# Optimization experiments

Hardware: AMD Instinct MI355X
Metric: run time of the kernel (lower is better)

The kernel has to match this reference:

```python
import jax, jax.numpy as jnp
import numpy as np

TOKENS = 16384
IN_F = 2048
OUT_F = 2048
RANK = 32
GROUP = 64          # int4 scale group size
PAD = 256           # token padding multiple used by the fused activation quantizer
QMAX = 7.0          # signed int4 symmetric quantization


def setup_inputs() -> dict:
    key = jax.random.key(0)
    ks = jax.random.split(key, 7)
    x = jax.random.normal(ks[0], (TOKENS, IN_F), dtype=jnp.float32)
    # packed int4 weights: two signed nibbles per int8 lane
    qweight = jax.random.randint(ks[1], (OUT_F, IN_F // 2), -128, 128, dtype=jnp.int8)
    # per-group weight scales [in//group, out], strictly positive
    wscales = jnp.abs(jax.random.normal(ks[2], (IN_F // GROUP, OUT_F), dtype=jnp.float32)) * 0.01 + 1e-4
    # activation smoothing factors, positive and near 1
    smooth_factor = jnp.abs(jax.random.normal(ks[3], (IN_F,), dtype=jnp.float32)) * 0.5 + 0.75
    bias = jax.random.normal(ks[4], (OUT_F,), dtype=jnp.float32) * 0.01
    proj_down = jax.random.normal(ks[5], (IN_F, RANK), dtype=jnp.float32) * 0.02
    proj_up = jax.random.normal(ks[6], (OUT_F, RANK), dtype=jnp.float32) * 0.02
    return {"x": x, "qweight": qweight, "wscales": wscales,
            "smooth_factor": smooth_factor, "bias": bias,
            "proj_down": proj_down, "proj_up": proj_up}


def _unpack_int4(qweight):
    # low nibble = even input channel, high nibble = odd input channel; arithmetic shifts keep sign
    low = jnp.right_shift(jnp.left_shift(qweight, 4), 4)
    high = jnpp = jnp.right_shift(qweight, 4)
    w = jnp.stack([low, high], axis=-1).reshape(qweight.shape[0], qweight.shape[1] * 2)
    return w.astype(jnp.float32)  # [out, in], values in [-8, 7]


def _forward(x, qweight, wscales, smooth_factor, bias, proj_down, proj_up):
    T = x.shape[0]
    t_pad = ((T + PAD - 1) // PAD) * PAD
    # activation smoothing
    xs = x / smooth_factor
    xs_p = jnp.pad(xs, ((0, t_pad - T), (0, 0)))
    # per-token per-64-group symmetric int4 activation quantization
    xg = xs_p.reshape(t_pad, IN_F // GROUP, GROUP)
    amax = jnp.max(jnp.abs(xg), axis=-1)                       # [Tp, G]
    ascales = jnp.where(amax > 0, amax / QMAX, jnp.float32(1.0))
    qx = jnp.clip(jnp.round(xg / ascales[..., None]), -8.0, 7.0)
    xdq = (qx * ascales[..., None]).reshape(t_pad, IN_F)       # dequantized activations
    # dequantize packed int4 weights with per-group scales
    w = _unpack_int4(qweight)                                  # [out, in]
    wdq = (w.reshape(OUT_F, IN_F // GROUP, GROUP) * wscales.T[:, :, None]).reshape(OUT_F, IN_F)
    # packed GEMM (dequantized equivalent) + fused low-rank residual + bias
    y = xdq @ wdq.T                                            # [Tp, out]
    y = y + (xs_p @ proj_down) @ proj_up.T + bias
    return y[:T]


def reference(x, qweight, wscales, smooth_factor, bias, proj_down, proj_up):
    return _forward(x, qweight, wscales, smooth_factor, bias, proj_down, proj_up)
```

## Files before the change

### kernel.cpp

```cpp
#include <hip/hip_runtime.h>

#define TOKENS 16384
#define INF 2048
#define OUTF 2048
#define NGROUP 32
#define RANK 32
#define BM 128
#define BN 128

typedef int   int32x4  __attribute__((ext_vector_type(4)));
typedef int   int32x2  __attribute__((ext_vector_type(2)));
typedef float floatx4  __attribute__((ext_vector_type(4)));
typedef short bf16x8   __attribute__((ext_vector_type(8)));

typedef __attribute__((address_space(1))) const void gconst_t;
typedef __attribute__((address_space(3))) void ldsv_t;

__device__ __forceinline__ void gload_lds16(const void* g, void* l) {
  __builtin_amdgcn_global_load_lds((gconst_t*)g, (ldsv_t*)l, 16, 0, 0);
}

__device__ __forceinline__ unsigned short f2bf(float f) {
  unsigned u = __float_as_uint(f);
  unsigned r = (u + 0x7FFFu + ((u >> 16) & 1u)) >> 16;
  return (unsigned short)r;
}

__device__ __forceinline__ unsigned unp2(int e0, int e1) {
  int l0 = ((int)((unsigned)e0 << 28)) >> 28;
  int h0 = ((int)((unsigned)e0 << 24)) >> 28;
  int l1 = ((int)((unsigned)e1 << 28)) >> 28;
  int h1 = ((int)((unsigned)e1 << 24)) >> 28;
  return (l0 & 0xFF) | ((h0 & 0xFF) << 8) | ((l1 & 0xFF) << 16) | ((h1 & 0xFF) << 24);
}

__global__ __launch_bounds__(256) void unpack_kernel(const int* __restrict__ qw,
                                                     signed char* __restrict__ wq8) {
  int idx = blockIdx.x * 256 + threadIdx.x;
  const int4* src = (const int4*)qw;
  int4 v0 = src[idx * 2 + 0];
  int4 v1 = src[idx * 2 + 1];
  int4 out;
  out.x = (int)unp2(v0.x, v0.y);
  out.y = (int)unp2(v0.z, v0.w);
  out.z = (int)unp2(v1.x, v1.y);
  out.w = (int)unp2(v1.z, v1.w);
  *(int4*)(wq8 + (size_t)idx * 16) = out;
}

__global__ __launch_bounds__(256) void prep_pdT(const float* __restrict__ pd,
                                                unsigned short* __restrict__ pdT) {
  int idx = blockIdx.x * 256 + threadIdx.x;
  int r = idx >> 11, c = idx & 2047;
  pdT[idx] = f2bf(pd[(size_t)c * RANK + r]);
}

__global__ __launch_bounds__(256) void quant_kernel(
    const float* __restrict__ x, const float* __restrict__ smooth,
    const unsigned short* __restrict__ pdT,
    signed char* __restrict__ qx8, float* __restrict__ ascalesT,
    float* __restrict__ tdown) {
  __shared__ char lds[32768];
  int tid = threadIdx.x, lane = tid & 63, wid = tid >> 6;
  int t0 = blockIdx.x * 32;
  int mi = wid >> 1, ni = wid & 1;
  floatx4 acc = {0.f, 0.f, 0.f, 0.f};

  floatx4 xv[8];
  floatx4 sm;
  int32x4 pv[4];

  auto issue_loads = [&](int kc) {
    const float* xb = x + (size_t)(t0 + wid * 8) * INF + kc * 256 + lane * 4;
#pragma unroll
    for (int r = 0; r < 8; ++r) xv[r] = *(const floatx4*)(xb + r * INF);
    sm = *(const floatx4*)(smooth + kc * 256 + lane * 4);
#pragma unroll
    for (int q = 0; q < 4; ++q) {
      int flat = tid + q * 256;
      int row = flat >> 5, c16 = flat & 31;
      pv[q] = *(const int32x4*)((const char*)pdT + (size_t)row * 4096 + kc * 512 + c16 * 16);
    }
  };

  issue_loads(0);

  for (int kc = 0; kc < 8; ++kc) {
    floatx4 rsm;
    rsm[0] = 1.0f / sm[0]; rsm[1] = 1.0f / sm[1];
    rsm[2] = 1.0f / sm[2]; rsm[3] = 1.0f / sm[3];
#pragma unroll
    for (int q = 0; q < 4; ++q) {
      int flat = tid + q * 256;
      int row = flat >> 5, c16 = flat & 31;
      int byte = (row * 512 + c16 * 16) ^ ((row & 7) << 4);
      *(int32x4*)(lds + 16384 + byte) = pv[q];
    }
#pragma unroll
    for (int r = 0; r < 8; ++r) {
      floatx4 xs;
      xs[0] = xv[r][0] * rsm[0]; xs[1] = xv[r][1] * rsm[1];
      xs[2] = xv[r][2] * rsm[2]; xs[3] = xv[r][3] * rsm[3];
      float m4 = fmaxf(fmaxf(fabsf(xs[0]), fabsf(xs[1])),
                       fmaxf(fabsf(xs[2]), fabsf(xs[3])));
      m4 = fmaxf(m4, __shfl_xor(m4, 1, 64));
      m4 = fmaxf(m4, __shfl_xor(m4, 2, 64));
      m4 = fmaxf(m4, __shfl_xor(m4, 4, 64));
      m4 = fmaxf(m4, __shfl_xor(m4, 8, 64));
      float ascale = m4 > 0.f ? m4 / 7.0f : 1.0f;
      float rq = 1.0f / ascale;
      int tok = t0 + wid * 8 + r;
      if ((lane & 15) == 0)
        ascalesT[(size_t)(kc * 4 + (lane >> 4)) * TOKENS + tok] = ascale;
      int pk = 0;
#pragma unroll
      for (int b = 0; b < 4; ++b) {
        float qf = fminf(7.f, fmaxf(-8.f, rintf(xs[b] * rq)));
        pk |= ((int)qf & 0xFF) << (8 * b);
      }
      *(int*)(qx8 + (size_t)tok * INF + kc * 256 + lane * 4) = pk;
      unsigned lo = (unsigned)f2bf(xs[0]) | ((unsigned)f2bf(xs[1]) << 16);
      unsigned hi = (unsigned)f2bf(xs[2]) | ((unsigned)f2bf(xs[3]) << 16);
      int lrow = wid * 8 + r;
      int xbyte = (lrow * 512 + lane * 8) ^ ((lrow & 7) << 4);
      int32x2 wv; wv[0] = (int)lo; wv[1] = (int)hi;
      *(int32x2*)(lds + xbyte) = wv;
    }
    __syncthreads();
    if (kc + 1 < 8) issue_loads(kc + 1);
#pragma unroll
    for (int ks = 0; ks < 8; ++ks) {
      int arow = mi * 16 + (lane & 15);
      int ab = (arow * 512 + ks * 64 + ((lane >> 4) << 4)) ^ ((arow & 7) << 4);
      bf16x8 av = *(const bf16x8*)(lds + ab);
      int brow = ni * 16 + (lane & 15);
      int bb = (brow * 512 + ks * 64 + ((lane >> 4) << 4)) ^ ((brow & 7) << 4);
      bf16x8 bv = *(const bf16x8*)(lds + 16384 + bb);
      acc = __builtin_amdgcn_mfma_f32_16x16x32_bf16(av, bv, acc, 0, 0, 0);
    }
    __syncthreads();
  }

  int trow = t0 + mi * 16 + ((lane >> 4) << 2);
  int col = ni * 16 + (lane & 15);
#pragma unroll
  for (int r = 0; r < 4; ++r)
    tdown[(size_t)(trow + r) * RANK + col] = acc[r];
}

__global__ __launch_bounds__(256, 3) void gemm_kernel(
    const signed char* __restrict__ qx8, const signed char* __restrict__ wq8,
    const float* __restrict__ ascalesT, const float* __restrict__ wscales,
    const float* __restrict__ tdown, const float* __restrict__ pu,
    const float* __restrict__ bias, float* __restrict__ y) {
  __shared__ char smem[49152];

  int tid = threadIdx.x;
  int lane = tid & 63;
  int wid = tid >> 6;
  int wr = wid >> 1, wc = wid & 1;
  int o0 = blockIdx.x * BN;
  int t0 = blockIdx.y * BM;

  floatx4 acc[4][4];
#pragma unroll
  for (int m = 0; m < 4; ++m)
#pragma unroll
    for (int n = 0; n < 4; ++n) acc[m][n] = (floatx4){0.f, 0.f, 0.f, 0.f};

  auto stage = [&](int g) {
    int bufb = (g % 3) * 16384;
#pragma unroll
    for (int i = 0; i < 2; ++i) {
      int c = tid + i * 256;
      int row = c >> 2;
      int l = (c & 3) ^ ((row >> 1) & 3);
      gload_lds16(qx8 + (size_t)(t0 + row) * INF + g * 64 + l * 16,
                  smem + bufb + (wid + i * 4) * 1024);
      gload_lds16(wq8 + (size_t)(o0 + row) * INF + g * 64 + l * 16,
                  smem + bufb + 8192 + (wid + i * 4) * 1024);
    }
  };

  int aoff[4], boff[4];
#pragma unroll
  for (int m = 0; m < 4; ++m) {
    int arow = (wr << 6) + (m << 4) + (lane & 15);
    aoff[m] = arow * 64 + ((((lane >> 4)) ^ ((arow >> 1) & 3)) << 4);
    int brow = (wc << 6) + (m << 4) + (lane & 15);
    boff[m] = 8192 + brow * 64 + ((((lane >> 4)) ^ ((brow >> 1) & 3)) << 4);
  }

  const float* asp = ascalesT + t0 + (wr << 6) + ((lane >> 4) << 2);
  const float* wsp = wscales + o0 + (wc << 6) + (lane & 15);

  floatx4 asv_pf[4];
  float wsv_pf[4];
  auto scales_pf = [&](int g) {
#pragma unroll
    for (int m = 0; m < 4; ++m)
      asv_pf[m] = *(const floatx4*)(asp + (size_t)g * TOKENS + (m << 4));
#pragma unroll
    for (int n = 0; n < 4; ++n)
      wsv_pf[n] = wsp[(size_t)g * OUTF + (n << 4)];
  };

  scales_pf(0);
  stage(0);
  stage(1);

  for (int g = 0; g < NGROUP; ++g) {
    if (g == 0)               asm volatile("s_waitcnt vmcnt(4)" ::: "memory");
    else if (g == NGROUP - 1) asm volatile("s_waitcnt vmcnt(8)" ::: "memory");
    else                      asm volatile("s_waitcnt vmcnt(12)" ::: "memory");
    __builtin_amdgcn_s_barrier();
    __builtin_amdgcn_sched_barrier(0);

    floatx4 asv[4];
    float wsv[4];
#pragma unroll
    for (int m = 0; m < 4; ++m) asv[m] = asv_pf[m];
#pragma unroll
    for (int n = 0; n < 4; ++n) wsv[n] = wsv_pf[n];

    if (g + 1 < NGROUP) scales_pf(g + 1);
    if (g + 2 < NGROUP) stage(g + 2);

    int bufb = (g % 3) * 16384;
    int32x4 af[4], bf_[4];
#pragma unroll
    for (int m = 0; m < 4; ++m) af[m] = *(const int32x4*)(smem + bufb + aoff[m]);
#pragma unroll
    for (int n = 0; n < 4; ++n) bf_[n] = *(const int32x4*)(smem + bufb + boff[n]);

    __builtin_amdgcn_s_setprio(1);
#pragma unroll
    for (int m = 0; m < 4; ++m)
#pragma unroll
      for (int n = 0; n < 4; ++n) {
        int32x4 zero = {0, 0, 0, 0};
        int32x4 d = __builtin_amdgcn_mfma_i32_16x16x64_i8(af[m], bf_[n], zero, 0, 0, 0);
        floatx4 sc;
        sc[0] = asv[m][0] * wsv[n]; sc[1] = asv[m][1] * wsv[n];
        sc[2] = asv[m][2] * wsv[n]; sc[3] = asv[m][3] * wsv[n];
        acc[m][n] += __builtin_convertvector(d, floatx4) * sc;
      }
    __builtin_amdgcn_s_setprio(0);
  }

  __syncthreads();

  unsigned short* td_lds = (unsigned short*)smem;
  unsigned short* pu_lds = (unsigned short*)(smem + 8192);
  {
    int row = tid >> 1, h = (tid & 1) * 16;
    const float* ts = tdown + (size_t)(t0 + row) * RANK + h;
    const float* ps = pu + (size_t)(o0 + row) * RANK + h;
    unsigned tw[8], pw[8];
#pragma unroll
    for (int q = 0; q < 4; ++q) {
      float4 v = *(const float4*)(ts + q * 4);
      tw[q * 2 + 0] = (unsigned)f2bf(v.x) | ((unsigned)f2bf(v.y) << 16);
      tw[q * 2 + 1] = (unsigned)f2bf(v.z) | ((unsigned)f2bf(v.w) << 16);
      float4 p = *(const float4*)(ps + q * 4);
      pw[q * 2 + 0] = (unsigned)f2bf(p.x) | ((unsigned)f2bf(p.y) << 16);
      pw[q * 2 + 1] = (unsigned)f2bf(p.z) | ((unsigned)f2bf(p.w) << 16);
    }
    int4 s0, s1;
    s0.x = (int)tw[0]; s0.y = (int)tw[1]; s0.z = (int)tw[2]; s0.w = (int)tw[3];
    s1.x = (int)tw[4]; s1.y = (int)tw[5]; s1.z = (int)tw[6]; s1.w = (int)tw[7];
    *(int4*)(td_lds + row * 32 + h) = s0;
    *(int4*)(td_lds + row * 32 + h + 8) = s1;
    s0.x = (int)pw[0]; s0.y = (int)pw[1]; s0.z = (int)pw[2]; s0.w = (int)pw[3];
    s1.x = (int)pw[4]; s1.y = (int)pw[5]; s1.z = (int)pw[6]; s1.w = (int)pw[7];
    *(int4*)(pu_lds + row * 32 + h) = s0;
    *(int4*)(pu_lds + row * 32 + h + 8) = s1;
  }
  __syncthreads();

  bf16x8 ta[4], pb4[4];
  int koff8 = (lane >> 4) << 3;
#pragma unroll
  for (int m = 0; m < 4; ++m)
    ta[m] = *(const bf16x8*)&td_lds[((wr << 6) + (m << 4) + (lane & 15)) * 32 + koff8];
#pragma unroll
  for (int n = 0; n < 4; ++n)
    pb4[n] = *(const bf16x8*)&pu_lds[((wc << 6) + (n << 4) + (lane & 15)) * 32 + koff8];

#pragma unroll
  for (int n = 0; n < 4; ++n) {
    int oc = o0 + (wc << 6) + (n << 4) + (lane & 15);
    float bv = bias[oc];
#pragma unroll
    for (int m = 0; m < 4; ++m) {
      floatx4 c = acc[m][n];
      c = __builtin_amdgcn_mfma_f32_16x16x32_bf16(ta[m], pb4[n], c, 0, 0, 0);
#pragma unroll
      for (int r = 0; r < 4; ++r) {
        int tr = t0 + (wr << 6) + (m << 4) + ((lane >> 4) << 2) + r;
        y[(size_t)tr * OUTF + oc] = c[r] + bv;
      }
    }
  }
}

extern "C" void kernel_launch(void* const* d_in, const int* in_sizes, int n_in,
                              void* d_out, int out_size, void* d_ws, size_t ws_size,
                              hipStream_t stream) {
  const float* x      = (const float*)d_in[0];
  const int*   qw     = (const int*)d_in[1];
  const float* wsc    = (const float*)d_in[2];
  const float* smooth = (const float*)d_in[3];
  const float* bias   = (const float*)d_in[4];
  const float* pd     = (const float*)d_in[5];
  const float* pu     = (const float*)d_in[6];
  float* y = (float*)d_out;

  char* ws = (char*)d_ws;
  signed char* qx8 = (signed char*)ws;
  signed char* wq8 = (signed char*)(ws + 33554432);
  float* ascalesT  = (float*)(ws + 33554432 + 4194304);
  float* tdown     = (float*)(ws + 33554432 + 4194304 + 2097152);
  unsigned short* pdT = (unsigned short*)((char*)d_out + (64u << 20));

  unpack_kernel<<<1024, 256, 0, stream>>>(qw, wq8);
  prep_pdT<<<256, 256, 0, stream>>>(pd, pdT);
  quant_kernel<<<TOKENS / 32, 256, 0, stream>>>(x, smooth, pdT, qx8, ascalesT, tdown);
  gemm_kernel<<<dim3(OUTF / BN, TOKENS / BM), 256, 0, stream>>>(
      qx8, wq8, ascalesT, wsc, tdown, pu, bias, y);
}
```

Before: 218.9 us.

## Replace int8 MFMA with pre-dequantized fp16 GEMM and split tokens in halves

Activations and weights are dequantized to fp16 in the prep kernels, with the group scales folded in, so the main GEMM runs fp16 MFMA that accumulate straight into the float accumulators. This removes the per-group scale loads and the int-to-float rescale after every int8 MFMA, but it doubles operand bytes and the number of K steps (64 steps of 32 elements instead of 32 groups). The token dimension is processed in two halves so the fp16 activation buffer fits in the existing workspace, and the GEMM grid is remapped to a 1D swizzled order for better L2 locality. fp16 rounding of the dequantized values could change numerics slightly.

```diff
diff --git a/kernel.cpp b/kernel.cpp
--- a/kernel.cpp
+++ b/kernel.cpp
@@ -1,17 +1,19 @@
 #include <hip/hip_runtime.h>
 
 #define TOKENS 16384
+#define THALF 8192
 #define INF 2048
 #define OUTF 2048
-#define NGROUP 32
 #define RANK 32
 #define BM 128
 #define BN 128
+#define NKSTEP 64
 
 typedef int   int32x4  __attribute__((ext_vector_type(4)));
 typedef int   int32x2  __attribute__((ext_vector_type(2)));
 typedef float floatx4  __attribute__((ext_vector_type(4)));
 typedef short bf16x8   __attribute__((ext_vector_type(8)));
+typedef _Float16 f16x8 __attribute__((ext_vector_type(8)));
 
 typedef __attribute__((address_space(1))) const void gconst_t;
 typedef __attribute__((address_space(3))) void ldsv_t;
@@ -26,26 +28,29 @@
   return (unsigned short)r;
 }
 
-__device__ __forceinline__ unsigned unp2(int e0, int e1) {
-  int l0 = ((int)((unsigned)e0 << 28)) >> 28;
-  int h0 = ((int)((unsigned)e0 << 24)) >> 28;
-  int l1 = ((int)((unsigned)e1 << 28)) >> 28;
-  int h1 = ((int)((unsigned)e1 << 24)) >> 28;
-  return (l0 & 0xFF) | ((h0 & 0xFF) << 8) | ((l1 & 0xFF) << 16) | ((h1 & 0xFF) << 24);
-}
-
 __global__ __launch_bounds__(256) void unpack_kernel(const int* __restrict__ qw,
-                                                     signed char* __restrict__ wq8) {
+                                                     const float* __restrict__ wsc,
+                                                     _Float16* __restrict__ wdq) {
   int idx = blockIdx.x * 256 + threadIdx.x;
-  const int4* src = (const int4*)qw;
-  int4 v0 = src[idx * 2 + 0];
-  int4 v1 = src[idx * 2 + 1];
-  int4 out;
-  out.x = (int)unp2(v0.x, v0.y);
-  out.y = (int)unp2(v0.z, v0.w);
-  out.z = (int)unp2(v1.x, v1.y);
-  out.w = (int)unp2(v1.z, v1.w);
-  *(int4*)(wq8 + (size_t)idx * 16) = out;
+  int o = idx >> 6;
+  int ch = idx & 63;
+  float ws = wsc[(size_t)(ch >> 1) * OUTF + o];
+  const int4* src = (const int4*)qw + (size_t)idx * 4;
+  _Float16* dst = wdq + (size_t)o * INF + ch * 32;
+#pragma unroll
+  for (int q = 0; q < 4; ++q) {
+    int4 v = src[q];
+    int e[4] = {v.x, v.y, v.z, v.w};
+    alignas(16) _Float16 h[8];
+#pragma unroll
+    for (int j = 0; j < 4; ++j) {
+      int lo = ((int)((unsigned)e[j] << 28)) >> 28;
+      int hi = ((int)((unsigned)e[j] << 24)) >> 28;
+      h[2 * j]     = (_Float16)((float)lo * ws);
+      h[2 * j + 1] = (_Float16)((float)hi * ws);
+    }
+    *(int4*)(dst + q * 8) = *(const int4*)h;
+  }
 }
 
 __global__ __launch_bounds__(256) void prep_pdT(const float* __restrict__ pd,
@@ -58,11 +63,10 @@
 __global__ __launch_bounds__(256) void quant_kernel(
     const float* __restrict__ x, const float* __restrict__ smooth,
     const unsigned short* __restrict__ pdT,
-    signed char* __restrict__ qx8, float* __restrict__ ascalesT,
-    float* __restrict__ tdown) {
+    _Float16* __restrict__ xdq, float* __restrict__ tdown, int tbase) {
   __shared__ char lds[32768];
   int tid = threadIdx.x, lane = tid & 63, wid = tid >> 6;
-  int t0 = blockIdx.x * 32;
+  int t0rel = blockIdx.x * 32;
   int mi = wid >> 1, ni = wid & 1;
   floatx4 acc = {0.f, 0.f, 0.f, 0.f};
 
@@ -71,7 +75,7 @@
   int32x4 pv[4];
 
   auto issue_loads = [&](int kc) {
-    const float* xb = x + (size_t)(t0 + wid * 8) * INF + kc * 256 + lane * 4;
+    const float* xb = x + (size_t)(tbase + t0rel + wid * 8) * INF + kc * 256 + lane * 4;
 #pragma unroll
     for (int r = 0; r < 8; ++r) xv[r] = *(const floatx4*)(xb + r * INF);
     sm = *(const floatx4*)(smooth + kc * 256 + lane * 4);
@@ -109,16 +113,15 @@
       m4 = fmaxf(m4, __shfl_xor(m4, 8, 64));
       float ascale = m4 > 0.f ? m4 / 7.0f : 1.0f;
       float rq = 1.0f / ascale;
-      int tok = t0 + wid * 8 + r;
-      if ((lane & 15) == 0)
-        ascalesT[(size_t)(kc * 4 + (lane >> 4)) * TOKENS + tok] = ascale;
-      int pk = 0;
+      int tokrel = t0rel + wid * 8 + r;
+      alignas(8) _Float16 hq[4];
 #pragma unroll
       for (int b = 0; b < 4; ++b) {
         float qf = fminf(7.f, fmaxf(-8.f, rintf(xs[b] * rq)));
-        pk |= ((int)qf & 0xFF) << (8 * b);
+        hq[b] = (_Float16)(qf * ascale);
       }
-      *(int*)(qx8 + (size_t)tok * INF + kc * 256 + lane * 4) = pk;
+      *(int32x2*)((char*)xdq + ((size_t)tokrel * INF + kc * 256 + lane * 4) * 2) =
+          *(const int32x2*)hq;
       unsigned lo = (unsigned)f2bf(xs[0]) | ((unsigned)f2bf(xs[1]) << 16);
       unsigned hi = (unsigned)f2bf(xs[2]) | ((unsigned)f2bf(xs[3]) << 16);
       int lrow = wid * 8 + r;
@@ -141,7 +144,7 @@
     __syncthreads();
   }
 
-  int trow = t0 + mi * 16 + ((lane >> 4) << 2);
+  int trow = tbase + t0rel + mi * 16 + ((lane >> 4) << 2);
   int col = ni * 16 + (lane & 15);
 #pragma unroll
   for (int r = 0; r < 4; ++r)
@@ -149,18 +152,21 @@
 }
 
 __global__ __launch_bounds__(256, 3) void gemm_kernel(
-    const signed char* __restrict__ qx8, const signed char* __restrict__ wq8,
-    const float* __restrict__ ascalesT, const float* __restrict__ wscales,
+    const _Float16* __restrict__ xdq, const _Float16* __restrict__ wdq,
     const float* __restrict__ tdown, const float* __restrict__ pu,
-    const float* __restrict__ bias, float* __restrict__ y) {
+    const float* __restrict__ bias, float* __restrict__ y, int tbase) {
   __shared__ char smem[49152];
 
   int tid = threadIdx.x;
   int lane = tid & 63;
   int wid = tid >> 6;
   int wr = wid >> 1, wc = wid & 1;
-  int o0 = blockIdx.x * BN;
-  int t0 = blockIdx.y * BM;
+
+  int s = blockIdx.x;
+  int s2 = (s & 7) * 128 + (s >> 3);
+  int o0 = (s2 & 15) * BN;
+  int t0rel = (s2 >> 4) * BM;
+  int t0abs = tbase + t0rel;
 
   floatx4 acc[4][4];
 #pragma unroll
@@ -175,9 +181,9 @@
       int c = tid + i * 256;
       int row = c >> 2;
       int l = (c & 3) ^ ((row >> 1) & 3);
-      gload_lds16(qx8 + (size_t)(t0 + row) * INF + g * 64 + l * 16,
+      gload_lds16((const char*)xdq + (size_t)(t0rel + row) * (INF * 2) + g * 64 + l * 16,
                   smem + bufb + (wid + i * 4) * 1024);
-      gload_lds16(wq8 + (size_t)(o0 + row) * INF + g * 64 + l * 16,
+      gload_lds16((const char*)wdq + (size_t)(o0 + row) * (INF * 2) + g * 64 + l * 16,
                   smem + bufb + 8192 + (wid + i * 4) * 1024);
     }
   };
@@ -191,60 +197,30 @@
     boff[m] = 8192 + brow * 64 + ((((lane >> 4)) ^ ((brow >> 1) & 3)) << 4);
   }
 
-  const float* asp = ascalesT + t0 + (wr << 6) + ((lane >> 4) << 2);
-  const float* wsp = wscales + o0 + (wc << 6) + (lane & 15);
-
-  floatx4 asv_pf[4];
-  float wsv_pf[4];
-  auto scales_pf = [&](int g) {
-#pragma unroll
-    for (int m = 0; m < 4; ++m)
-      asv_pf[m] = *(const floatx4*)(asp + (size_t)g * TOKENS + (m << 4));
-#pragma unroll
-    for (int n = 0; n < 4; ++n)
-      wsv_pf[n] = wsp[(size_t)g * OUTF + (n << 4)];
-  };
-
-  scales_pf(0);
   stage(0);
   stage(1);
 
-  for (int g = 0; g < NGROUP; ++g) {
-    if (g == 0)               asm volatile("s_waitcnt vmcnt(4)" ::: "memory");
-    else if (g == NGROUP - 1) asm volatile("s_waitcnt vmcnt(8)" ::: "memory");
-    else                      asm volatile("s_waitcnt vmcnt(12)" ::: "memory");
+  for (int g = 0; g < NKSTEP; ++g) {
+    if (g == NKSTEP - 1) asm volatile("s_waitcnt vmcnt(0)" ::: "memory");
+    else                 asm volatile("s_waitcnt vmcnt(4)" ::: "memory");
     __builtin_amdgcn_s_barrier();
     __builtin_amdgcn_sched_barrier(0);
 
-    floatx4 asv[4];
-    float wsv[4];
-#pragma unroll
-    for (int m = 0; m < 4; ++m) asv[m] = asv_pf[m];
-#pragma unroll
-    for (int n = 0; n < 4; ++n) wsv[n] = wsv_pf[n];
-
-    if (g + 1 < NGROUP) scales_pf(g + 1);
-    if (g + 2 < NGROUP) stage(g + 2);
+    if (g + 2 < NKSTEP) stage(g + 2);
 
     int bufb = (g % 3) * 16384;
-    int32x4 af[4], bf_[4];
-#pragma unroll
-    for (int m = 0; m < 4; ++m) af[m] = *(const int32x4*)(smem + bufb + aoff[m]);
-#pragma unroll
-    for (int n = 0; n < 4; ++n) bf_[n] = *(const int32x4*)(smem + bufb + boff[n]);
+    f16x8 af[4], bf_[4];
+#pragma unroll
+    for (int m = 0; m < 4; ++m) af[m] = *(const f16x8*)(smem + bufb + aoff[m]);
+#pragma unroll
+    for (int n = 0; n < 4; ++n) bf_[n] = *(const f16x8*)(smem + bufb + boff[n]);
 
     __builtin_amdgcn_s_setprio(1);
 #pragma unroll
     for (int m = 0; m < 4; ++m)
 #pragma unroll
-      for (int n = 0; n < 4; ++n) {
-        int32x4 zero = {0, 0, 0, 0};
-        int32x4 d = __builtin_amdgcn_mfma_i32_16x16x64_i8(af[m], bf_[n], zero, 0, 0, 0);
-        floatx4 sc;
-        sc[0] = asv[m][0] * wsv[n]; sc[1] = asv[m][1] * wsv[n];
-        sc[2] = asv[m][2] * wsv[n]; sc[3] = asv[m][3] * wsv[n];
-        acc[m][n] += __builtin_convertvector(d, floatx4) * sc;
-      }
+      for (int n = 0; n < 4; ++n)
+        acc[m][n] = __builtin_amdgcn_mfma_f32_16x16x32_f16(af[m], bf_[n], acc[m][n], 0, 0, 0);
     __builtin_amdgcn_s_setprio(0);
   }
 
@@ -254,7 +230,7 @@
   unsigned short* pu_lds = (unsigned short*)(smem + 8192);
   {
     int row = tid >> 1, h = (tid & 1) * 16;
-    const float* ts = tdown + (size_t)(t0 + row) * RANK + h;
+    const float* ts = tdown + (size_t)(t0abs + row) * RANK + h;
     const float* ps = pu + (size_t)(o0 + row) * RANK + h;
     unsigned tw[8], pw[8];
 #pragma unroll
@@ -297,7 +273,7 @@
       c = __builtin_amdgcn_mfma_f32_16x16x32_bf16(ta[m], pb4[n], c, 0, 0, 0);
 #pragma unroll
       for (int r = 0; r < 4; ++r) {
-        int tr = t0 + (wr << 6) + (m << 4) + ((lane >> 4) << 2) + r;
+        int tr = t0abs + (wr << 6) + (m << 4) + ((lane >> 4) << 2) + r;
         y[(size_t)tr * OUTF + oc] = c[r] + bv;
       }
     }
@@ -317,15 +293,17 @@
   float* y = (float*)d_out;
 
   char* ws = (char*)d_ws;
-  signed char* qx8 = (signed char*)ws;
-  signed char* wq8 = (signed char*)(ws + 33554432);
-  float* ascalesT  = (float*)(ws + 33554432 + 4194304);
-  float* tdown     = (float*)(ws + 33554432 + 4194304 + 2097152);
+  _Float16* xdq = (_Float16*)ws;
+  _Float16* wdq = (_Float16*)(ws + 33554432);
+  float* tdown  = (float*)(ws + 33554432 + 8388608);
   unsigned short* pdT = (unsigned short*)((char*)d_out + (64u << 20));
 
-  unpack_kernel<<<1024, 256, 0, stream>>>(qw, wq8);
+  unpack_kernel<<<512, 256, 0, stream>>>(qw, wsc, wdq);
   prep_pdT<<<256, 256, 0, stream>>>(pd, pdT);
-  quant_kernel<<<TOKENS / 32, 256, 0, stream>>>(x, smooth, pdT, qx8, ascalesT, tdown);
-  gemm_kernel<<<dim3(OUTF / BN, TOKENS / BM), 256, 0, stream>>>(
-      qx8, wq8, ascalesT, wsc, tdown, pu, bias, y);
-}
+  for (int c = 0; c < 2; ++c) {
+    int tbase = c * THALF;
+    quant_kernel<<<THALF / 32, 256, 0, stream>>>(x, smooth, pdT, xdq, tdown, tbase);
+    gemm_kernel<<<(OUTF / BN) * (THALF / BM), 256, 0, stream>>>(
+        xdq, wdq, tdown, pu, bias, y, tbase);
+  }
+}
```

New measurement: 266.1 us. 21.6% more time.

## Enlarge GEMM tile to 256x256 with 512 threads, XCD-aware mapping, fused prep kernels

Applied to the files above, without the earlier changes.

The int8 GEMM tile grows from 128x128 with 4 waves to 256x256 with 8 waves. Each wave now computes 128x64 in two half-passes so register pressure stays bounded. Staging drops from a triple-buffered pipeline to a double buffer with a full vmcnt(0) wait, and scale prefetch is replaced by in-loop loads. Blocks are remapped to a 1D grid so that tiles sharing data land on the same XCD, and the two prep kernels are merged into one launch. The larger tile cuts global and L2 traffic per FLOP, but it risks lower occupancy (512 blocks, 2 per CU) and less latency hiding from the shallower pipeline.

```diff
diff --git a/kernel.cpp b/kernel.cpp
--- a/kernel.cpp
+++ b/kernel.cpp
@@ -3,10 +3,10 @@
 #define TOKENS 16384
 #define INF 2048
 #define OUTF 2048
-#define NGROUP 32
 #define RANK 32
-#define BM 128
-#define BN 128
+#define BM 256
+#define BN 256
+#define NPER 32
 
 typedef int   int32x4  __attribute__((ext_vector_type(4)));
 typedef int   int32x2  __attribute__((ext_vector_type(2)));
@@ -34,25 +34,27 @@
   return (l0 & 0xFF) | ((h0 & 0xFF) << 8) | ((l1 & 0xFF) << 16) | ((h1 & 0xFF) << 24);
 }
 
-__global__ __launch_bounds__(256) void unpack_kernel(const int* __restrict__ qw,
-                                                     signed char* __restrict__ wq8) {
-  int idx = blockIdx.x * 256 + threadIdx.x;
-  const int4* src = (const int4*)qw;
-  int4 v0 = src[idx * 2 + 0];
-  int4 v1 = src[idx * 2 + 1];
-  int4 out;
-  out.x = (int)unp2(v0.x, v0.y);
-  out.y = (int)unp2(v0.z, v0.w);
-  out.z = (int)unp2(v1.x, v1.y);
-  out.w = (int)unp2(v1.z, v1.w);
-  *(int4*)(wq8 + (size_t)idx * 16) = out;
-}
-
-__global__ __launch_bounds__(256) void prep_pdT(const float* __restrict__ pd,
-                                                unsigned short* __restrict__ pdT) {
-  int idx = blockIdx.x * 256 + threadIdx.x;
-  int r = idx >> 11, c = idx & 2047;
-  pdT[idx] = f2bf(pd[(size_t)c * RANK + r]);
+__global__ __launch_bounds__(256) void prep_kernel(const int* __restrict__ qw,
+                                                   signed char* __restrict__ wq8,
+                                                   const float* __restrict__ pd,
+                                                   unsigned short* __restrict__ pdT) {
+  int b = blockIdx.x;
+  if (b < 1024) {
+    int idx = b * 256 + threadIdx.x;
+    const int4* src = (const int4*)qw;
+    int4 v0 = src[idx * 2 + 0];
+    int4 v1 = src[idx * 2 + 1];
+    int4 out;
+    out.x = (int)unp2(v0.x, v0.y);
+    out.y = (int)unp2(v0.z, v0.w);
+    out.z = (int)unp2(v1.x, v1.y);
+    out.w = (int)unp2(v1.z, v1.w);
+    *(int4*)(wq8 + (size_t)idx * 16) = out;
+  } else {
+    int idx = (b - 1024) * 256 + threadIdx.x;
+    int r = idx >> 11, c = idx & 2047;
+    pdT[idx] = f2bf(pd[(size_t)c * RANK + r]);
+  }
 }
 
 __global__ __launch_bounds__(256) void quant_kernel(
@@ -148,110 +150,127 @@
     tdown[(size_t)(trow + r) * RANK + col] = acc[r];
 }
 
-__global__ __launch_bounds__(256, 3) void gemm_kernel(
+__global__ __launch_bounds__(512, 2) void gemm_kernel(
     const signed char* __restrict__ qx8, const signed char* __restrict__ wq8,
     const float* __restrict__ ascalesT, const float* __restrict__ wscales,
     const float* __restrict__ tdown, const float* __restrict__ pu,
     const float* __restrict__ bias, float* __restrict__ y) {
-  __shared__ char smem[49152];
+  __shared__ char smem[65536];
 
   int tid = threadIdx.x;
   int lane = tid & 63;
   int wid = tid >> 6;
-  int wr = wid >> 1, wc = wid & 1;
-  int o0 = blockIdx.x * BN;
-  int t0 = blockIdx.y * BM;
-
-  floatx4 acc[4][4];
-#pragma unroll
-  for (int m = 0; m < 4; ++m)
+  int wm = wid >> 2, wn = wid & 3;
+
+  int s = blockIdx.x;
+  int xcd = s & 7, idx = s >> 3;
+  int o0 = (((xcd & 3) << 1) + (idx & 1)) * BN;
+  int t0 = ((xcd >> 2) * 32 + (idx >> 1)) * BM;
+
+  floatx4 acc[8][4];
+#pragma unroll
+  for (int m = 0; m < 8; ++m)
 #pragma unroll
     for (int n = 0; n < 4; ++n) acc[m][n] = (floatx4){0.f, 0.f, 0.f, 0.f};
 
   auto stage = [&](int g) {
-    int bufb = (g % 3) * 16384;
+    int bufb = (g & 1) * 32768;
 #pragma unroll
     for (int i = 0; i < 2; ++i) {
-      int c = tid + i * 256;
-      int row = c >> 2;
-      int l = (c & 3) ^ ((row >> 1) & 3);
-      gload_lds16(qx8 + (size_t)(t0 + row) * INF + g * 64 + l * 16,
-                  smem + bufb + (wid + i * 4) * 1024);
-      gload_lds16(wq8 + (size_t)(o0 + row) * INF + g * 64 + l * 16,
-                  smem + bufb + 8192 + (wid + i * 4) * 1024);
+      int f = i * 512 + tid;
+      int row = f >> 2, sl = (f & 3) ^ ((row >> 1) & 3);
+      gload_lds16(qx8 + (size_t)(t0 + row) * INF + g * 64 + sl * 16,
+                  smem + bufb + i * 8192 + wid * 1024);
+    }
+#pragma unroll
+    for (int i = 0; i < 2; ++i) {
+      int f = i * 512 + tid;
+      int row = f >> 2, sl = (f & 3) ^ ((row >> 1) & 3);
+      gload_lds16(wq8 + (size_t)(o0 + row) * INF + g * 64 + sl * 16,
+                  smem + bufb + 16384 + i * 8192 + wid * 1024);
     }
   };
 
-  int aoff[4], boff[4];
-#pragma unroll
-  for (int m = 0; m < 4; ++m) {
-    int arow = (wr << 6) + (m << 4) + (lane & 15);
-    aoff[m] = arow * 64 + ((((lane >> 4)) ^ ((arow >> 1) & 3)) << 4);
-    int brow = (wc << 6) + (m << 4) + (lane & 15);
-    boff[m] = 8192 + brow * 64 + ((((lane >> 4)) ^ ((brow >> 1) & 3)) << 4);
-  }
-
-  const float* asp = ascalesT + t0 + (wr << 6) + ((lane >> 4) << 2);
-  const float* wsp = wscales + o0 + (wc << 6) + (lane & 15);
-
-  floatx4 asv_pf[4];
-  float wsv_pf[4];
-  auto scales_pf = [&](int g) {
-#pragma unroll
-    for (int m = 0; m < 4; ++m)
-      asv_pf[m] = *(const floatx4*)(asp + (size_t)g * TOKENS + (m << 4));
-#pragma unroll
-    for (int n = 0; n < 4; ++n)
-      wsv_pf[n] = wsp[(size_t)g * OUTF + (n << 4)];
-  };
-
-  scales_pf(0);
+  int l = lane & 15;
+  int sw = (l >> 1) & 3;
+  int abase = wm * 8192 + l * 64 + (((lane >> 4) ^ sw) << 4);
+  int bbase = 16384 + wn * 4096 + l * 64 + (((lane >> 4) ^ sw) << 4);
+
+  const float* asp = ascalesT + t0 + wm * 128 + ((lane >> 4) << 2);
+  const float* wsp = wscales + o0 + wn * 64 + l;
+
   stage(0);
-  stage(1);
-
-  for (int g = 0; g < NGROUP; ++g) {
-    if (g == 0)               asm volatile("s_waitcnt vmcnt(4)" ::: "memory");
-    else if (g == NGROUP - 1) asm volatile("s_waitcnt vmcnt(8)" ::: "memory");
-    else                      asm volatile("s_waitcnt vmcnt(12)" ::: "memory");
+
+  for (int g = 0; g < NPER; ++g) {
+    asm volatile("s_waitcnt vmcnt(0)" ::: "memory");
     __builtin_amdgcn_s_barrier();
     __builtin_amdgcn_sched_barrier(0);
 
-    floatx4 asv[4];
+    int bufb = (g & 1) * 32768;
+    int32x4 bfr[4], afr[4];
+#pragma unroll
+    for (int n = 0; n < 4; ++n) bfr[n] = *(const int32x4*)(smem + bufb + bbase + n * 1024);
+#pragma unroll
+    for (int m = 0; m < 4; ++m) afr[m] = *(const int32x4*)(smem + bufb + abase + m * 1024);
+
+    if (g + 1 < NPER) stage(g + 1);
+
+    floatx4 asv[8];
     float wsv[4];
 #pragma unroll
-    for (int m = 0; m < 4; ++m) asv[m] = asv_pf[m];
-#pragma unroll
-    for (int n = 0; n < 4; ++n) wsv[n] = wsv_pf[n];
-
-    if (g + 1 < NGROUP) scales_pf(g + 1);
-    if (g + 2 < NGROUP) stage(g + 2);
-
-    int bufb = (g % 3) * 16384;
-    int32x4 af[4], bf_[4];
-#pragma unroll
-    for (int m = 0; m < 4; ++m) af[m] = *(const int32x4*)(smem + bufb + aoff[m]);
-#pragma unroll
-    for (int n = 0; n < 4; ++n) bf_[n] = *(const int32x4*)(smem + bufb + boff[n]);
-
+    for (int m = 0; m < 8; ++m) asv[m] = *(const floatx4*)(asp + (size_t)g * TOKENS + m * 16);
+#pragma unroll
+    for (int n = 0; n < 4; ++n) wsv[n] = wsp[(size_t)g * OUTF + n * 16];
+
+    asm volatile("s_waitcnt lgkmcnt(0)" ::: "memory");
+    __builtin_amdgcn_sched_barrier(0);
     __builtin_amdgcn_s_setprio(1);
 #pragma unroll
-    for (int m = 0; m < 4; ++m)
+    for (int m = 0; m < 4; ++m) {
+      int32x4 d[4];
 #pragma unroll
       for (int n = 0; n < 4; ++n) {
         int32x4 zero = {0, 0, 0, 0};
-        int32x4 d = __builtin_amdgcn_mfma_i32_16x16x64_i8(af[m], bf_[n], zero, 0, 0, 0);
+        d[n] = __builtin_amdgcn_mfma_i32_16x16x64_i8(afr[m], bfr[n], zero, 0, 0, 0);
+      }
+#pragma unroll
+      for (int n = 0; n < 4; ++n) {
         floatx4 sc;
         sc[0] = asv[m][0] * wsv[n]; sc[1] = asv[m][1] * wsv[n];
         sc[2] = asv[m][2] * wsv[n]; sc[3] = asv[m][3] * wsv[n];
-        acc[m][n] += __builtin_convertvector(d, floatx4) * sc;
-      }
+        acc[m][n] += __builtin_convertvector(d[n], floatx4) * sc;
+      }
+    }
     __builtin_amdgcn_s_setprio(0);
+
+#pragma unroll
+    for (int m = 0; m < 4; ++m) afr[m] = *(const int32x4*)(smem + bufb + abase + (4 + m) * 1024);
+    asm volatile("s_waitcnt lgkmcnt(0)" ::: "memory");
+    __builtin_amdgcn_sched_barrier(0);
+    __builtin_amdgcn_s_setprio(1);
+#pragma unroll
+    for (int m = 0; m < 4; ++m) {
+      int32x4 d[4];
+#pragma unroll
+      for (int n = 0; n < 4; ++n) {
+        int32x4 zero = {0, 0, 0, 0};
+        d[n] = __builtin_amdgcn_mfma_i32_16x16x64_i8(afr[m], bfr[n], zero, 0, 0, 0);
+      }
+#pragma unroll
+      for (int n = 0; n < 4; ++n) {
+        floatx4 sc;
+        sc[0] = asv[4 + m][0] * wsv[n]; sc[1] = asv[4 + m][1] * wsv[n];
+        sc[2] = asv[4 + m][2] * wsv[n]; sc[3] = asv[4 + m][3] * wsv[n];
+        acc[4 + m][n] += __builtin_convertvector(d[n], floatx4) * sc;
+      }
+    }
+    __builtin_amdgcn_s_setprio(0);
   }
 
   __syncthreads();
 
   unsigned short* td_lds = (unsigned short*)smem;
-  unsigned short* pu_lds = (unsigned short*)(smem + 8192);
+  unsigned short* pu_lds = (unsigned short*)(smem + 16384);
   {
     int row = tid >> 1, h = (tid & 1) * 16;
     const float* ts = tdown + (size_t)(t0 + row) * RANK + h;
@@ -278,26 +297,26 @@
   }
   __syncthreads();
 
-  bf16x8 ta[4], pb4[4];
+  bf16x8 ta[8], pb4[4];
   int koff8 = (lane >> 4) << 3;
 #pragma unroll
-  for (int m = 0; m < 4; ++m)
-    ta[m] = *(const bf16x8*)&td_lds[((wr << 6) + (m << 4) + (lane & 15)) * 32 + koff8];
+  for (int m = 0; m < 8; ++m)
+    ta[m] = *(const bf16x8*)&td_lds[((wm << 7) + (m << 4) + (lane & 15)) * 32 + koff8];
 #pragma unroll
   for (int n = 0; n < 4; ++n)
-    pb4[n] = *(const bf16x8*)&pu_lds[((wc << 6) + (n << 4) + (lane & 15)) * 32 + koff8];
+    pb4[n] = *(const bf16x8*)&pu_lds[((wn << 6) + (n << 4) + (lane & 15)) * 32 + koff8];
 
 #pragma unroll
   for (int n = 0; n < 4; ++n) {
-    int oc = o0 + (wc << 6) + (n << 4) + (lane & 15);
+    int oc = o0 + (wn << 6) + (n << 4) + (lane & 15);
     float bv = bias[oc];
 #pragma unroll
-    for (int m = 0; m < 4; ++m) {
+    for (int m = 0; m < 8; ++m) {
       floatx4 c = acc[m][n];
       c = __builtin_amdgcn_mfma_f32_16x16x32_bf16(ta[m], pb4[n], c, 0, 0, 0);
 #pragma unroll
       for (int r = 0; r < 4; ++r) {
-        int tr = t0 + (wr << 6) + (m << 4) + ((lane >> 4) << 2) + r;
+        int tr = t0 + (wm << 7) + (m << 4) + ((lane >> 4) << 2) + r;
         y[(size_t)tr * OUTF + oc] = c[r] + bv;
       }
     }
@@ -323,9 +342,8 @@
   float* tdown     = (float*)(ws + 33554432 + 4194304 + 2097152);
   unsigned short* pdT = (unsigned short*)((char*)d_out + (64u << 20));
 
-  unpack_kernel<<<1024, 256, 0, stream>>>(qw, wq8);
-  prep_pdT<<<256, 256, 0, stream>>>(pd, pdT);
+  prep_kernel<<<1280, 256, 0, stream>>>(qw, wq8, pd, pdT);
   quant_kernel<<<TOKENS / 32, 256, 0, stream>>>(x, smooth, pdT, qx8, ascalesT, tdown);
-  gemm_kernel<<<dim3(OUTF / BN, TOKENS / BM), 256, 0, stream>>>(
+  gemm_kernel<<<8 * (TOKENS / BM), 512, 0, stream>>>(
       qx8, wq8, ascalesT, wsc, tdown, pu, bias, y);
 }
```

New measurement: 232.5 us. +6.2%, slower.
